# Kernel optimization log

Measured on AMD Instinct MI355X. Metric: run time of the kernel, lower is better.

## Reference

```python
import jax, jax.numpy as jnp
import numpy as np

PAD = 0
B, S = 8, 256
V, E, H = 32000, 512, 1024


def setup_inputs() -> dict:
    key = jax.random.key(0)
    ks = jax.random.split(key, 8)
    s = lambda k, shape, fan: jax.random.normal(k, shape, dtype=jnp.float32) / np.sqrt(fan)
    return {
        "x": jax.random.randint(ks[0], (B, S), 0, V, dtype=jnp.int32),
        "emb_W": s(ks[1], (V, E), E),          # embedding table, shared with generator
        "W_ih": s(ks[2], (3 * H, E), E),        # GRU input->gates (r,z,n)
        "W_hh": s(ks[3], (3 * H, H), H),        # GRU hidden->gates
        "b_ih": jnp.zeros((3 * H,), jnp.float32),
        "b_hh": jnp.zeros((3 * H,), jnp.float32),
        "lin_W": s(ks[4], (E, H + E), H + E),   # linear_logit
        "lin_b": jnp.zeros((E,), jnp.float32),
    }


def _gru(emb, mask, W_ih, W_hh, b_ih, b_hh):
    # emb: [B,S,E], mask: [B,S] True at PAD. Returns ctx [B,S,H].
    gx = jnp.einsum('bse,ge->bsg', emb, W_ih) + b_ih  # [B,S,3H] precomputed input gates
    gx_t = jnp.swapaxes(gx, 0, 1)                      # [S,B,3H]
    m_t = jnp.swapaxes(mask, 0, 1)                     # [S,B]

    def step(h, inp):
        g_x, m = inp
        g_h = h @ W_hh.T + b_hh
        xr, xz, xn = jnp.split(g_x, 3, axis=-1)
        hr, hz, hn = jnp.split(g_h, 3, axis=-1)
        r = jax.nn.sigmoid(xr + hr)
        z = jax.nn.sigmoid(xz + hz)
        n = jnp.tanh(xn + r * hn)
        h_new = (1.0 - z) * n + z * h
        h = jnp.where(m[:, None], h, h_new)            # carry hidden through PAD steps
        out = jnp.where(m[:, None], 0.0, h)            # packed-seq outputs are 0 at PAD
        return h, out

    h0 = jnp.zeros((emb.shape[0], W_hh.shape[1]), emb.dtype)
    _, ctx = jax.lax.scan(step, h0, (gx_t, m_t))
    return jnp.swapaxes(ctx, 0, 1)                     # [B,S,H]


def reference(x, emb_W, W_ih, W_hh, b_ih, b_hh, lin_W, lin_b):
    mask = (x == PAD)
    emb = emb_W[x]                                     # [B,S,E]
    ctx = _gru(emb, mask, W_ih, W_hh, b_ih, b_hh)      # [B,S,H]
    feat = jnp.concatenate([ctx, emb], axis=-1)        # [B,S,H+E]
    logits = jnp.tanh(feat @ lin_W.T + lin_b)          # [B,S,E]
    scores = logits @ emb_W.T                          # [B,S,V] shared-weight generator
    return jax.nn.log_softmax(scores, axis=-1)
```

## Files before the change

### kernel.cpp

```cpp
#include <hip/hip_runtime.h>

typedef unsigned int u32;
typedef unsigned short u16;
typedef unsigned long long u64;
typedef __attribute__((ext_vector_type(8))) short short8;
typedef __attribute__((ext_vector_type(4))) float floatx4;

#define BB 8
#define SS 256
#define VV 32000
#define EE 512
#define HH 1024
#define GRU_BLOCKS 64
#define GRU_THREADS 192
#define NCHUNK 500

__device__ __forceinline__ float b2f(u16 h) {
  union { u32 u; float f; } c; c.u = ((u32)h) << 16; return c.f;
}
__device__ __forceinline__ u16 f2b_bits(u32 u) {
  return (u16)((u + 0x7FFFu + ((u >> 16) & 1u)) >> 16);
}
__device__ __forceinline__ u16 f2b(float f) {
  union { float f; u32 u; } c; c.f = f; return f2b_bits(c.u);
}

__global__ __launch_bounds__(256) void k_detect(const u32* __restrict__ w, int* __restrict__ dflag) {
  __shared__ int cnt;
  if (threadIdx.x == 0) cnt = 0;
  __syncthreads();
  int c = 0;
  for (int i = threadIdx.x; i < 8192; i += 256) {
    u32 e8 = (w[i] >> 7) & 0xFF;
    c += (e8 >= 100 && e8 <= 144);
  }
  atomicAdd(&cnt, c);
  __syncthreads();
  if (threadIdx.x == 0) dflag[0] = (cnt * 2 > 8192) ? 1 : 0;
}

__global__ __launch_bounds__(256) void k_conv(const void* __restrict__ src, u16* __restrict__ dst,
                                              int n, const int* __restrict__ dflag) {
  int i = (blockIdx.x * 256 + threadIdx.x) * 8;
  if (i >= n) return;
  if (dflag[0]) {
    *(uint4*)(dst + i) = *(const uint4*)((const u16*)src + i);
  } else {
    const float* s = (const float*)src + i;
    uint4 a = *(const uint4*)s, b = *(const uint4*)(s + 4);
    u32 w0 = ((u32)f2b_bits(a.y) << 16) | f2b_bits(a.x);
    u32 w1 = ((u32)f2b_bits(a.w) << 16) | f2b_bits(a.z);
    u32 w2 = ((u32)f2b_bits(b.y) << 16) | f2b_bits(b.x);
    u32 w3 = ((u32)f2b_bits(b.w) << 16) | f2b_bits(b.z);
    uint4 r; r.x = w0; r.y = w1; r.z = w2; r.w = w3;
    *(uint4*)(dst + i) = r;
  }
}

__global__ __launch_bounds__(256) void k_init(u32* h_tag, int* dflag, int setflag) {
  int t = threadIdx.x;
  for (int i = t; i < 2 * 8192; i += 256) h_tag[i] = 0;
  if (t == 0 && setflag >= 0) dflag[0] = setflag;
}

__global__ __launch_bounds__(64) void k_gather(const int* __restrict__ x,
                                               const u16* __restrict__ embW,
                                               u16* __restrict__ emb,
                                               u16* __restrict__ feat) {
  int row = blockIdx.x, l = threadIdx.x;
  int tok = x[row];
  uint4 v = ((const uint4*)(embW + (size_t)tok * EE))[l];
  ((uint4*)(emb + (size_t)row * EE))[l] = v;
  ((uint4*)(feat + (size_t)row * 1536 + HH))[l] = v;
}

template <int KTOT>
__device__ __forceinline__ void gemm_core(const u16* __restrict__ A, int lda,
                                          const u16* __restrict__ Bm, int ldb,
                                          int m0, int n0, floatx4 acc[4][4]) {
  __shared__ __align__(16) u16 As[128 * 64];
  __shared__ __align__(16) u16 Bs[128 * 64];
  const int tid = threadIdx.x;
  const int lane = tid & 63, w = tid >> 6;
  const int wm = w & 1, wn = w >> 1;
  const int col16 = lane & 15, quad = lane >> 4;
  floatx4 z = {0.f, 0.f, 0.f, 0.f};
  for (int i = 0; i < 4; i++)
    for (int j = 0; j < 4; j++) acc[i][j] = z;

  for (int k0 = 0; k0 < KTOT; k0 += 64) {
#pragma unroll
    for (int i = 0; i < 4; i++) {
      int c = tid + i * 256;
      int r = c >> 3, off = (c & 7) * 8;
      *(uint4*)&As[r * 64 + off] = *(const uint4*)&A[(size_t)(m0 + r) * lda + k0 + off];
      *(uint4*)&Bs[r * 64 + off] = *(const uint4*)&Bm[(size_t)(n0 + r) * ldb + k0 + off];
    }
    __syncthreads();
#pragma unroll
    for (int kk = 0; kk < 2; kk++) {
      short8 af[4], bf[4];
#pragma unroll
      for (int i = 0; i < 4; i++) {
        af[i] = *(const short8*)&As[(wm * 64 + i * 16 + col16) * 64 + kk * 32 + quad * 8];
        bf[i] = *(const short8*)&Bs[(wn * 64 + i * 16 + col16) * 64 + kk * 32 + quad * 8];
      }
#pragma unroll
      for (int i = 0; i < 4; i++)
#pragma unroll
        for (int j = 0; j < 4; j++)
          acc[i][j] = __builtin_amdgcn_mfma_f32_16x16x32_bf16(af[i], bf[j], acc[i][j], 0, 0, 0);
    }
    __syncthreads();
  }
}

__global__ __launch_bounds__(256) void k_gx(const u16* __restrict__ emb,
                                            const u16* __restrict__ W_ih,
                                            const u16* __restrict__ b_ih,
                                            float* __restrict__ gx2) {
  floatx4 acc[4][4];
  int bm = blockIdx.x, bn = blockIdx.y;
  gemm_core<EE>(emb, EE, W_ih, EE, bm * 128, bn * 128, acc);
  const int tid = threadIdx.x, lane = tid & 63, w = tid >> 6;
  const int wm = w & 1, wn = w >> 1, col16 = lane & 15, quad = lane >> 4;
#pragma unroll
  for (int j = 0; j < 4; j++) {
    int g = bn * 128 + wn * 64 + j * 16 + col16;
    float bias = b2f(b_ih[g]);
    int grp = g >> 10, colh = g & 1023;
    int gb = colh >> 4, slot = grp * 16 + (colh & 15);
#pragma unroll
    for (int i = 0; i < 4; i++)
#pragma unroll
      for (int e = 0; e < 4; e++) {
        int row = bm * 128 + wm * 64 + i * 16 + quad * 4 + e;
        int b = row >> 8, s = row & 255;
        gx2[((size_t)(s * 64 + gb) * 48 + slot) * 8 + b] = acc[i][j][e] + bias;
      }
  }
}

__global__ __launch_bounds__(GRU_THREADS) void k_gru(const u16* __restrict__ W_hh,
                                                     const u16* __restrict__ b_hh,
                                                     const int* __restrict__ x,
                                                     const float* __restrict__ gx2,
                                                     u32* __restrict__ h_tag,
                                                     u16* __restrict__ feat) {
  __shared__ __align__(16) u16 h_lds[16][1032];
  __shared__ float gh[3][16][8];
  __shared__ float hold[16][8];
  __shared__ float bhh[48];
  __shared__ int x_s[2048];

  const int tid = threadIdx.x;
  const int lane = tid & 63, w = tid >> 6;
  const int blk = blockIdx.x, hc = blk * 16;
  const int col16 = lane & 15, quad = lane >> 4;

  for (int i = tid; i < 16 * 1032; i += GRU_THREADS) ((u16*)h_lds)[i] = 0;
  for (int i = tid; i < 2048; i += GRU_THREADS) x_s[i] = x[i];
  if (tid < 128) hold[tid & 15][tid >> 4] = 0.f;
  if (tid < 48) bhh[tid] = b2f(b_hh[(tid >> 4) * HH + hc + (tid & 15)]);

  short8 Wf[32];
  {
    int grow = w * HH + hc + col16;
    const u16* wp = W_hh + (size_t)grow * HH + quad * 8;
#pragma unroll
    for (int t = 0; t < 32; t++) Wf[t] = *(const short8*)(wp + t * 32);
  }
  __syncthreads();

  const int cj = tid & 15, cb = tid >> 4;
#pragma unroll 1
  for (int s = 0; s < SS; s++) {
    float xr = 0.f, xz = 0.f, xn = 0.f;
    if (tid < 128) {
      const float* gp = gx2 + (size_t)(s * 64 + blk) * 384;
      xr = gp[cj * 8 + cb];
      xz = gp[128 + cj * 8 + cb];
      xn = gp[256 + cj * 8 + cb];
    }
    {
      const u64* hb = (const u64*)(h_tag + (size_t)(s & 1) * 8192);
      const u32 want = (u32)(s & 0xFFFF);
      u64 vals[22];
      u32 pend = 0;
#pragma unroll
      for (int i = 0; i < 22; i++)
        if (tid + i * GRU_THREADS < 4096) pend |= 1u << i;
      int guard = 0;
      while (pend) {
#pragma unroll
        for (int i = 0; i < 22; i++)
          if (pend & (1u << i))
            vals[i] = __hip_atomic_load(hb + (tid + i * GRU_THREADS),
                                        __ATOMIC_RELAXED, __HIP_MEMORY_SCOPE_AGENT);
#pragma unroll
        for (int i = 0; i < 22; i++)
          if (pend & (1u << i)) {
            u64 v = vals[i];
            if ((u32)(v & 0xFFFFu) == want && ((u32)(v >> 32) & 0xFFFFu) == want) {
              int pr = tid + i * GRU_THREADS;
              u32 packed = ((u32)(v >> 16) & 0xFFFFu) | ((u32)(v >> 48) << 16);
              *(u32*)&h_lds[pr >> 9][(pr & 511) * 2] = packed;
              pend &= ~(1u << i);
            }
          }
        if (pend) {
          __builtin_amdgcn_s_sleep(1);
          if (++guard > (1 << 14)) break;
        }
      }
    }
    __syncthreads();
    {
      const u16* hp = &h_lds[col16][quad * 8];
      floatx4 a0 = {0.f, 0.f, 0.f, 0.f}, a1 = {0.f, 0.f, 0.f, 0.f};
#pragma unroll
      for (int t = 0; t < 32; t += 2) {
        short8 f0 = *(const short8*)(hp + t * 32);
        short8 f1 = *(const short8*)(hp + t * 32 + 32);
        a0 = __builtin_amdgcn_mfma_f32_16x16x32_bf16(f0, Wf[t], a0, 0, 0, 0);
        a1 = __builtin_amdgcn_mfma_f32_16x16x32_bf16(f1, Wf[t + 1], a1, 0, 0, 0);
      }
      a0 += a1;
      if (quad < 2) {
#pragma unroll
        for (int e = 0; e < 4; e++) gh[w][col16][quad * 4 + e] = a0[e];
      }
    }
    __syncthreads();
    if (tid < 128) {
      float hr = gh[0][cj][cb] + bhh[cj];
      float hz = gh[1][cj][cb] + bhh[16 + cj];
      float hn = gh[2][cj][cb] + bhh[32 + cj];
      float r = 1.f / (1.f + __expf(-(xr + hr)));
      float z = 1.f / (1.f + __expf(-(xz + hz)));
      float tn = xn + r * hn;
      float n = 1.f - 2.f / (1.f + __expf(2.f * tn));
      float ho = hold[cj][cb];
      float hnew = (1.f - z) * n + z * ho;
      int pad = (x_s[cb * SS + s] == 0);
      if (pad) hnew = ho;
      hold[cj][cb] = hnew;
      u16 hb16 = f2b(hnew);
      u32 tw = ((u32)hb16 << 16) | (u32)((s + 1) & 0xFFFF);
      __hip_atomic_store(h_tag + (size_t)((s + 1) & 1) * 8192 + cb * 1024 + hc + cj, tw,
                         __ATOMIC_RELAXED, __HIP_MEMORY_SCOPE_AGENT);
      feat[(size_t)(cb * SS + s) * 1536 + hc + cj] = pad ? (u16)0 : hb16;
    }
  }
}

__global__ __launch_bounds__(256) void k_lin(const u16* __restrict__ feat,
                                             const u16* __restrict__ lin_W,
                                             const u16* __restrict__ lin_b,
                                             u16* __restrict__ logits) {
  floatx4 acc[4][4];
  int bm = blockIdx.x, bn = blockIdx.y;
  gemm_core<1536>(feat, 1536, lin_W, 1536, bm * 128, bn * 128, acc);
  const int tid = threadIdx.x, lane = tid & 63, w = tid >> 6;
  const int wm = w & 1, wn = w >> 1, col16 = lane & 15, quad = lane >> 4;
#pragma unroll
  for (int j = 0; j < 4; j++) {
    int col = bn * 128 + wn * 64 + j * 16 + col16;
    float bias = b2f(lin_b[col]);
#pragma unroll
    for (int i = 0; i < 4; i++)
#pragma unroll
      for (int e = 0; e < 4; e++) {
        int row = bm * 128 + wm * 64 + i * 16 + quad * 4 + e;
        logits[(size_t)row * EE + col] = f2b(tanhf(acc[i][j][e] + bias));
      }
  }
}

__global__ __launch_bounds__(256) void k_scores(const u16* __restrict__ logits,
                                                const u16* __restrict__ embW,
                                                void* __restrict__ outv,
                                                float* __restrict__ partial,
                                                const int* __restrict__ dflag) {
  floatx4 acc[4][4];
  int bm = blockIdx.x, bn = blockIdx.y;
  gemm_core<EE>(logits, EE, embW, EE, bm * 128, bn * 128, acc);
  const int tid = threadIdx.x, lane = tid & 63, w = tid >> 6;
  const int wm = w & 1, wn = w >> 1, col16 = lane & 15, quad = lane >> 4;
  const int bf = dflag[0];
  u16* out16 = (u16*)outv;
  float* out32 = (float*)outv;
#pragma unroll
  for (int i = 0; i < 4; i++) {
#pragma unroll
    for (int e = 0; e < 4; e++) {
      int row = bm * 128 + wm * 64 + i * 16 + quad * 4 + e;
      size_t ob = (size_t)row * VV + bn * 128 + wn * 64;
      float sl = 0.f;
#pragma unroll
      for (int j = 0; j < 4; j++) {
        float v = acc[i][j][e];
        if (bf) out16[ob + j * 16 + col16] = f2b(v);
        else    out32[ob + j * 16 + col16] = v;
        sl += __expf(v);
      }
      sl += __shfl_xor(sl, 1, 64);
      sl += __shfl_xor(sl, 2, 64);
      sl += __shfl_xor(sl, 4, 64);
      sl += __shfl_xor(sl, 8, 64);
      if (col16 == 0) partial[(size_t)row * NCHUNK + bn * 2 + wn] = sl;
    }
  }
}

__global__ __launch_bounds__(64) void k_lse(const float* __restrict__ partial,
                                            float* __restrict__ lse) {
  int row = blockIdx.x, lane = threadIdx.x;
  float s = 0.f;
  for (int c = lane; c < NCHUNK; c += 64) s += partial[(size_t)row * NCHUNK + c];
#pragma unroll
  for (int d = 32; d >= 1; d >>= 1) s += __shfl_xor(s, d, 64);
  if (lane == 0) lse[row] = logf(s);
}

__global__ __launch_bounds__(256) void k_fix(void* __restrict__ outv,
                                             const float* __restrict__ lse,
                                             const int* __restrict__ dflag) {
  int g = blockIdx.x * 256 + threadIdx.x;
  if (dflag[0]) {
    if (g >= 8192000) return;
    u16* out = (u16*)outv;
    int row = g / 4000;
    float l = lse[row];
    uint4 v = ((const uint4*)out)[g];
    u32 a[4] = {v.x, v.y, v.z, v.w};
#pragma unroll
    for (int k = 0; k < 4; k++) {
      float lo = b2f((u16)(a[k] & 0xffff)) - l;
      float hi = b2f((u16)(a[k] >> 16)) - l;
      a[k] = ((u32)f2b(hi) << 16) | (u32)f2b(lo);
    }
    uint4 r; r.x = a[0]; r.y = a[1]; r.z = a[2]; r.w = a[3];
    ((uint4*)out)[g] = r;
  } else {
    float* out = (float*)outv;
    int row = g / 8000;
    float l = lse[row];
    float4 v = ((const float4*)out)[g];
    v.x -= l; v.y -= l; v.z -= l; v.w -= l;
    ((float4*)out)[g] = v;
  }
}

extern "C" void kernel_launch(void* const* d_in, const int* in_sizes, int n_in,
                              void* d_out, int out_size, void* d_ws, size_t ws_size,
                              hipStream_t stream) {
  const int* x = (const int*)d_in[0];

  char* ws = (char*)d_ws;
  float* gx2     = (float*)(ws);
  u16*   feat    = (u16*)(ws + 25165824);
  u16*   emb     = (u16*)(ws + 31457280);
  u16*   logits  = (u16*)(ws + 33554432);
  u32*   h_tag   = (u32*)(ws + 35651584);
  float* partial = (float*)(ws + 35717120);
  float* lse     = (float*)(ws + 39813120);
  int*   dflag   = (int*)(ws + 39821312);
  u16*   embW_c  = (u16*)(ws + 39821568);
  u16*   Wih_c   = (u16*)(ws + 72589568);
  u16*   Whh_c   = (u16*)(ws + 75735296);
  u16*   linW_c  = (u16*)(ws + 82026752);
  u16*   bih_c   = (u16*)(ws + 83599616);
  u16*   bhh_c   = (u16*)(ws + 83605760);
  u16*   linb_c  = (u16*)(ws + 83611904);
  const size_t TOTAL_WS = 83612928;

  const u16 *embW, *W_ih, *W_hh, *b_ih, *b_hh, *lin_W, *lin_b;
  if (ws_size >= TOTAL_WS) {
    k_detect<<<1, 256, 0, stream>>>((const u32*)d_in[1], dflag);
    k_init<<<1, 256, 0, stream>>>(h_tag, dflag, -1);
    k_conv<<<8000, 256, 0, stream>>>(d_in[1], embW_c, VV * EE, dflag);
    k_conv<<<1536, 256, 0, stream>>>(d_in[3], Whh_c, 3 * HH * HH, dflag);
    k_conv<<<768,  256, 0, stream>>>(d_in[2], Wih_c, 3 * HH * EE, dflag);
    k_conv<<<384,  256, 0, stream>>>(d_in[6], linW_c, EE * (HH + EE), dflag);
    k_conv<<<2,    256, 0, stream>>>(d_in[4], bih_c, 3 * HH, dflag);
    k_conv<<<2,    256, 0, stream>>>(d_in[5], bhh_c, 3 * HH, dflag);
    k_conv<<<1,    256, 0, stream>>>(d_in[7], linb_c, EE, dflag);
    embW = embW_c; W_ih = Wih_c; W_hh = Whh_c; b_ih = bih_c;
    b_hh = bhh_c; lin_W = linW_c; lin_b = linb_c;
  } else {
    k_init<<<1, 256, 0, stream>>>(h_tag, dflag, 1);
    embW = (const u16*)d_in[1]; W_ih = (const u16*)d_in[2]; W_hh = (const u16*)d_in[3];
    b_ih = (const u16*)d_in[4]; b_hh = (const u16*)d_in[5];
    lin_W = (const u16*)d_in[6]; lin_b = (const u16*)d_in[7];
  }

  k_gather<<<2048, 64, 0, stream>>>(x, embW, emb, feat);
  k_gx<<<dim3(16, 24), 256, 0, stream>>>(emb, W_ih, b_ih, gx2);
  k_gru<<<GRU_BLOCKS, GRU_THREADS, 0, stream>>>(W_hh, b_hh, x, gx2, h_tag, feat);
  k_lin<<<dim3(16, 4), 256, 0, stream>>>(feat, lin_W, lin_b, logits);
  k_scores<<<dim3(16, 250), 256, 0, stream>>>(logits, embW, d_out, partial, dflag);
  k_lse<<<2048, 64, 0, stream>>>(partial, lse);
  k_fix<<<64000, 256, 0, stream>>>(d_out, lse, dflag);
}
```

Baseline: 1.912 ms.

## Add per-wavefront ready flags to GRU cross-block handoff and widen MFMA chains

Each GRU step now has every producer wavefront publish a step-counter flag after its tagged hidden-state stores. Consumers poll 128 flags with ballots and only load tagged h words from producers marked ready, instead of repeatedly loading all 22 tagged words per thread. The h_tag layout is re-indexed per producer wavefront, the s_sleep back-off is dropped, and the recurrent MFMA loop uses four independent accumulators. Risks: the flags buffer aliases the lse workspace, which is only safe because k_lse runs later. Ordering relies on relaxed atomics plus s_waitcnt, and spinning without sleep may add memory contention.

After: 2.465 ms. 1.29x slower.

```diff
diff --git a/kernel.cpp b/kernel.cpp
--- a/kernel.cpp
+++ b/kernel.cpp
@@ -57,9 +57,10 @@
   }
 }
 
-__global__ __launch_bounds__(256) void k_init(u32* h_tag, int* dflag, int setflag) {
+__global__ __launch_bounds__(256) void k_init(u32* h_tag, u32* flags, int* dflag, int setflag) {
   int t = threadIdx.x;
   for (int i = t; i < 2 * 8192; i += 256) h_tag[i] = 0;
+  if (t < 256) flags[t] = 0;
   if (t == 0 && setflag >= 0) dflag[0] = setflag;
 }
 
@@ -146,6 +147,7 @@
                                                      const int* __restrict__ x,
                                                      const float* __restrict__ gx2,
                                                      u32* __restrict__ h_tag,
+                                                     u32* __restrict__ flags,
                                                      u16* __restrict__ feat) {
   __shared__ __align__(16) u16 h_lds[16][1032];
   __shared__ float gh[3][16][8];
@@ -184,32 +186,47 @@
     }
     {
       const u64* hb = (const u64*)(h_tag + (size_t)(s & 1) * 8192);
+      const u32* flg = flags + (s & 1) * 128;
       const u32 want = (u32)(s & 0xFFFF);
-      u64 vals[22];
+      const u32 wflag = (u32)s;
       u32 pend = 0;
 #pragma unroll
       for (int i = 0; i < 22; i++)
         if (tid + i * GRU_THREADS < 4096) pend |= 1u << i;
       int guard = 0;
-      while (pend) {
-#pragma unroll
-        for (int i = 0; i < 22; i++)
-          if (pend & (1u << i))
-            vals[i] = __hip_atomic_load(hb + (tid + i * GRU_THREADS),
-                                        __ATOMIC_RELAXED, __HIP_MEMORY_SCOPE_AGENT);
+      while (__any((int)pend)) {
+        u32 f0 = __hip_atomic_load(flg + lane, __ATOMIC_RELAXED, __HIP_MEMORY_SCOPE_AGENT);
+        u32 f1 = __hip_atomic_load(flg + 64 + lane, __ATOMIC_RELAXED, __HIP_MEMORY_SCOPE_AGENT);
+        u64 m0 = __ballot(f0 >= wflag);
+        u64 m1 = __ballot(f1 >= wflag);
+        u64 vals[22];
+        u32 rdy = 0;
 #pragma unroll
         for (int i = 0; i < 22; i++)
           if (pend & (1u << i)) {
+            int c = tid + i * GRU_THREADS;
+            int pw = c >> 5;
+            u64 mm = (pw & 64) ? m1 : m0;
+            if ((mm >> (pw & 63)) & 1) {
+              vals[i] = __hip_atomic_load(hb + c, __ATOMIC_RELAXED, __HIP_MEMORY_SCOPE_AGENT);
+              rdy |= 1u << i;
+            }
+          }
+#pragma unroll
+        for (int i = 0; i < 22; i++)
+          if (rdy & (1u << i)) {
             u64 v = vals[i];
             if ((u32)(v & 0xFFFFu) == want && ((u32)(v >> 32) & 0xFFFFu) == want) {
-              int pr = tid + i * GRU_THREADS;
+              int c = tid + i * GRU_THREADS;
+              int pw = c >> 5, p31 = c & 31;
+              int b = (pw & 1) * 4 + (p31 >> 3);
+              int col = (pw >> 1) * 16 + (p31 & 7) * 2;
               u32 packed = ((u32)(v >> 16) & 0xFFFFu) | ((u32)(v >> 48) << 16);
-              *(u32*)&h_lds[pr >> 9][(pr & 511) * 2] = packed;
+              *(u32*)&h_lds[b][col] = packed;
               pend &= ~(1u << i);
             }
           }
         if (pend) {
-          __builtin_amdgcn_s_sleep(1);
           if (++guard > (1 << 14)) break;
         }
       }
@@ -218,14 +235,19 @@
     {
       const u16* hp = &h_lds[col16][quad * 8];
       floatx4 a0 = {0.f, 0.f, 0.f, 0.f}, a1 = {0.f, 0.f, 0.f, 0.f};
-#pragma unroll
-      for (int t = 0; t < 32; t += 2) {
+      floatx4 a2 = {0.f, 0.f, 0.f, 0.f}, a3 = {0.f, 0.f, 0.f, 0.f};
+#pragma unroll
+      for (int t = 0; t < 32; t += 4) {
         short8 f0 = *(const short8*)(hp + t * 32);
-        short8 f1 = *(const short8*)(hp + t * 32 + 32);
+        short8 f1 = *(const short8*)(hp + (t + 1) * 32);
+        short8 f2 = *(const short8*)(hp + (t + 2) * 32);
+        short8 f3 = *(const short8*)(hp + (t + 3) * 32);
         a0 = __builtin_amdgcn_mfma_f32_16x16x32_bf16(f0, Wf[t], a0, 0, 0, 0);
         a1 = __builtin_amdgcn_mfma_f32_16x16x32_bf16(f1, Wf[t + 1], a1, 0, 0, 0);
-      }
-      a0 += a1;
+        a2 = __builtin_amdgcn_mfma_f32_16x16x32_bf16(f2, Wf[t + 2], a2, 0, 0, 0);
+        a3 = __builtin_amdgcn_mfma_f32_16x16x32_bf16(f3, Wf[t + 3], a3, 0, 0, 0);
+      }
+      a0 += a1; a2 += a3; a0 += a2;
       if (quad < 2) {
 #pragma unroll
         for (int e = 0; e < 4; e++) gh[w][col16][quad * 4 + e] = a0[e];
@@ -247,8 +269,14 @@
       hold[cj][cb] = hnew;
       u16 hb16 = f2b(hnew);
       u32 tw = ((u32)hb16 << 16) | (u32)((s + 1) & 0xFFFF);
-      __hip_atomic_store(h_tag + (size_t)((s + 1) & 1) * 8192 + cb * 1024 + hc + cj, tw,
+      int pw = blk * 2 + (tid >> 6);
+      int idx = (pw << 6) | ((cb & 3) << 4) | cj;
+      __hip_atomic_store(h_tag + (size_t)((s + 1) & 1) * 8192 + idx, tw,
                          __ATOMIC_RELAXED, __HIP_MEMORY_SCOPE_AGENT);
+      asm volatile("s_waitcnt vmcnt(0)" ::: "memory");
+      if ((tid & 63) == 0)
+        __hip_atomic_store(flags + ((s + 1) & 1) * 128 + pw, (u32)(s + 1),
+                           __ATOMIC_RELAXED, __HIP_MEMORY_SCOPE_AGENT);
       feat[(size_t)(cb * SS + s) * 1536 + hc + cj] = pad ? (u16)0 : hb16;
     }
   }
@@ -365,6 +393,7 @@
   u32*   h_tag   = (u32*)(ws + 35651584);
   float* partial = (float*)(ws + 35717120);
   float* lse     = (float*)(ws + 39813120);
+  u32*   flags   = (u32*)(ws + 39813120);
   int*   dflag   = (int*)(ws + 39821312);
   u16*   embW_c  = (u16*)(ws + 39821568);
   u16*   Wih_c   = (u16*)(ws + 72589568);
@@ -378,7 +407,7 @@
   const u16 *embW, *W_ih, *W_hh, *b_ih, *b_hh, *lin_W, *lin_b;
   if (ws_size >= TOTAL_WS) {
     k_detect<<<1, 256, 0, stream>>>((const u32*)d_in[1], dflag);
-    k_init<<<1, 256, 0, stream>>>(h_tag, dflag, -1);
+    k_init<<<1, 256, 0, stream>>>(h_tag, flags, dflag, -1);
     k_conv<<<8000, 256, 0, stream>>>(d_in[1], embW_c, VV * EE, dflag);
     k_conv<<<1536, 256, 0, stream>>>(d_in[3], Whh_c, 3 * HH * HH, dflag);
     k_conv<<<768,  256, 0, stream>>>(d_in[2], Wih_c, 3 * HH * EE, dflag);
@@ -389,7 +418,7 @@
     embW = embW_c; W_ih = Wih_c; W_hh = Whh_c; b_ih = bih_c;
     b_hh = bhh_c; lin_W = linW_c; lin_b = linb_c;
   } else {
-    k_init<<<1, 256, 0, stream>>>(h_tag, dflag, 1);
+    k_init<<<1, 256, 0, stream>>>(h_tag, flags, dflag, 1);
     embW = (const u16*)d_in[1]; W_ih = (const u16*)d_in[2]; W_hh = (const u16*)d_in[3];
     b_ih = (const u16*)d_in[4]; b_hh = (const u16*)d_in[5];
     lin_W = (const u16*)d_in[6]; lin_b = (const u16*)d_in[7];
@@ -397,7 +426,7 @@
 
   k_gather<<<2048, 64, 0, stream>>>(x, embW, emb, feat);
   k_gx<<<dim3(16, 24), 256, 0, stream>>>(emb, W_ih, b_ih, gx2);
-  k_gru<<<GRU_BLOCKS, GRU_THREADS, 0, stream>>>(W_hh, b_hh, x, gx2, h_tag, feat);
+  k_gru<<<GRU_BLOCKS, GRU_THREADS, 0, stream>>>(W_hh, b_hh, x, gx2, h_tag, flags, feat);
   k_lin<<<dim3(16, 4), 256, 0, stream>>>(feat, lin_W, lin_b, logits);
   k_scores<<<dim3(16, 250), 256, 0, stream>>>(logits, embW, d_out, partial, dflag);
   k_lse<<<2048, 64, 0, stream>>>(partial, lse);
```

## Add per-block step flags to GRU grid sync and keep own hidden slice local

Applied to the files above, without the earlier changes.

Before loading the hidden state, each GRU block now spins on per-block step flags, one per peer block, so the polling of tagged hidden values should normally succeed on the first pass. The block writes its own hidden slice straight into LDS and skips re-reading it from global memory, and the s_sleep backoff is removed. The cost is an extra flag wait, a barrier and a flag store per step. The flags buffer sits at the same workspace offset as lse; that is safe only because lse is written later, in k_lse.

Measured after the change: 1.807 ms. 5.5% less time.

```diff
diff --git a/kernel.cpp b/kernel.cpp
--- a/kernel.cpp
+++ b/kernel.cpp
@@ -57,9 +57,10 @@
   }
 }
 
-__global__ __launch_bounds__(256) void k_init(u32* h_tag, int* dflag, int setflag) {
+__global__ __launch_bounds__(256) void k_init(u32* h_tag, u32* flags, int* dflag, int setflag) {
   int t = threadIdx.x;
   for (int i = t; i < 2 * 8192; i += 256) h_tag[i] = 0;
+  if (t < 128) flags[t] = 0;
   if (t == 0 && setflag >= 0) dflag[0] = setflag;
 }
 
@@ -146,6 +147,7 @@
                                                      const int* __restrict__ x,
                                                      const float* __restrict__ gx2,
                                                      u32* __restrict__ h_tag,
+                                                     u32* __restrict__ flags,
                                                      u16* __restrict__ feat) {
   __shared__ __align__(16) u16 h_lds[16][1032];
   __shared__ float gh[3][16][8];
@@ -182,14 +184,24 @@
       xz = gp[128 + cj * 8 + cb];
       xn = gp[256 + cj * 8 + cb];
     }
+    if (tid < 64 && tid != blk) {
+      const u32* fp = flags + (s & 1) * 64 + tid;
+      int guard = 0;
+      while (__hip_atomic_load(fp, __ATOMIC_RELAXED, __HIP_MEMORY_SCOPE_AGENT) != (u32)s) {
+        if (++guard > (1 << 20)) break;
+      }
+    }
+    __syncthreads();
     {
       const u64* hb = (const u64*)(h_tag + (size_t)(s & 1) * 8192);
       const u32 want = (u32)(s & 0xFFFF);
       u64 vals[22];
       u32 pend = 0;
 #pragma unroll
-      for (int i = 0; i < 22; i++)
-        if (tid + i * GRU_THREADS < 4096) pend |= 1u << i;
+      for (int i = 0; i < 22; i++) {
+        int pr = tid + i * GRU_THREADS;
+        if (pr < 4096 && ((pr & 511) >> 3) != blk) pend |= 1u << i;
+      }
       int guard = 0;
       while (pend) {
 #pragma unroll
@@ -209,7 +221,6 @@
             }
           }
         if (pend) {
-          __builtin_amdgcn_s_sleep(1);
           if (++guard > (1 << 14)) break;
         }
       }
@@ -249,8 +260,12 @@
       u32 tw = ((u32)hb16 << 16) | (u32)((s + 1) & 0xFFFF);
       __hip_atomic_store(h_tag + (size_t)((s + 1) & 1) * 8192 + cb * 1024 + hc + cj, tw,
                          __ATOMIC_RELAXED, __HIP_MEMORY_SCOPE_AGENT);
+      h_lds[cb][hc + cj] = hb16;
       feat[(size_t)(cb * SS + s) * 1536 + hc + cj] = pad ? (u16)0 : hb16;
     }
+    if (tid == 0)
+      __hip_atomic_store(flags + ((s + 1) & 1) * 64 + blk, (u32)(s + 1),
+                         __ATOMIC_RELAXED, __HIP_MEMORY_SCOPE_AGENT);
   }
 }
 
@@ -365,6 +380,7 @@
   u32*   h_tag   = (u32*)(ws + 35651584);
   float* partial = (float*)(ws + 35717120);
   float* lse     = (float*)(ws + 39813120);
+  u32*   flags   = (u32*)(ws + 39813120);
   int*   dflag   = (int*)(ws + 39821312);
   u16*   embW_c  = (u16*)(ws + 39821568);
   u16*   Wih_c   = (u16*)(ws + 72589568);
@@ -378,7 +394,7 @@
   const u16 *embW, *W_ih, *W_hh, *b_ih, *b_hh, *lin_W, *lin_b;
   if (ws_size >= TOTAL_WS) {
     k_detect<<<1, 256, 0, stream>>>((const u32*)d_in[1], dflag);
-    k_init<<<1, 256, 0, stream>>>(h_tag, dflag, -1);
+    k_init<<<1, 256, 0, stream>>>(h_tag, flags, dflag, -1);
     k_conv<<<8000, 256, 0, stream>>>(d_in[1], embW_c, VV * EE, dflag);
     k_conv<<<1536, 256, 0, stream>>>(d_in[3], Whh_c, 3 * HH * HH, dflag);
     k_conv<<<768,  256, 0, stream>>>(d_in[2], Wih_c, 3 * HH * EE, dflag);
@@ -389,7 +405,7 @@
     embW = embW_c; W_ih = Wih_c; W_hh = Whh_c; b_ih = bih_c;
     b_hh = bhh_c; lin_W = linW_c; lin_b = linb_c;
   } else {
-    k_init<<<1, 256, 0, stream>>>(h_tag, dflag, 1);
+    k_init<<<1, 256, 0, stream>>>(h_tag, flags, dflag, 1);
     embW = (const u16*)d_in[1]; W_ih = (const u16*)d_in[2]; W_hh = (const u16*)d_in[3];
     b_ih = (const u16*)d_in[4]; b_hh = (const u16*)d_in[5];
     lin_W = (const u16*)d_in[6]; lin_b = (const u16*)d_in[7];
@@ -397,7 +413,7 @@
 
   k_gather<<<2048, 64, 0, stream>>>(x, embW, emb, feat);
   k_gx<<<dim3(16, 24), 256, 0, stream>>>(emb, W_ih, b_ih, gx2);
-  k_gru<<<GRU_BLOCKS, GRU_THREADS, 0, stream>>>(W_hh, b_hh, x, gx2, h_tag, feat);
+  k_gru<<<GRU_BLOCKS, GRU_THREADS, 0, stream>>>(W_hh, b_hh, x, gx2, h_tag, flags, feat);
   k_lin<<<dim3(16, 4), 256, 0, stream>>>(feat, lin_W, lin_b, logits);
   k_scores<<<dim3(16, 250), 256, 0, stream>>>(logits, embW, d_out, partial, dflag);
   k_lse<<<2048, 64, 0, stream>>>(partial, lse);
```
